# Kernel tuning notes

Hardware: AMD Instinct MI355X
Metric: run time of the kernel (lower is better)

The kernel has to match this reference:

```python
import jax, jax.numpy as jnp
import numpy as np

B, N, C = 128, 320, 768
H = 12
T = 64    # template tokens (8x8)
S = 256   # search tokens (16x16)


def setup_inputs() -> dict:
    key = jax.random.key(0)
    k1, k2, k3, k4 = jax.random.split(key, 4)
    return {
        "x1": jax.random.normal(k1, (B, N, C), dtype=jnp.float32),
        "x2": jax.random.normal(k2, (B, N, C), dtype=jnp.float32),
        "qkv_w": jax.random.normal(k3, (3 * C, C), dtype=jnp.float32) * 0.02,
        "proj_w": jax.random.normal(k4, (C, C), dtype=jnp.float32) * 0.02,
        "proj_b": jnp.zeros((C,), dtype=jnp.float32),
    }


def reference(x1, x2, qkv_w, proj_w, proj_b):
    # concat template tokens from x1 with search tokens from x2
    x = jnp.concatenate([x1[:, :T, :], x2[:, T:, :]], axis=1)  # [B, N, C]
    b, n, c = x.shape
    d = c // H
    scale = d ** -0.5

    qkv = (x @ qkv_w.T).reshape(b, n, 3, H, d).transpose(2, 0, 3, 1, 4)  # [3,B,H,N,D]
    q, k, v = qkv[0], qkv[1], qkv[2]

    # template -> template self-attention
    q_mt, k_mt, v_mt = q[:, :, :T], k[:, :, :T], v[:, :, :T]
    attn_mt = jax.nn.softmax(jnp.einsum('bhtd,bhsd->bhts', q_mt, k_mt) * scale, axis=-1)
    x_mt = jnp.einsum('bhts,bhsd->bhtd', attn_mt, v_mt).transpose(0, 2, 1, 3).reshape(b, T, c)

    # search -> all cross+self attention
    q_s = q[:, :, T:]
    attn_s = jax.nn.softmax(jnp.einsum('bhqd,bhkd->bhqk', q_s, k) * scale, axis=-1)
    x_s = jnp.einsum('bhqk,bhkd->bhqd', attn_s, v).transpose(0, 2, 1, 3).reshape(b, S, c)

    out = jnp.concatenate([x_mt, x_s], axis=1) @ proj_w.T + proj_b
    return out
```

## Files before the change

### kernel.cpp

```cpp
#include <hip/hip_runtime.h>
#include <hip/hip_bf16.h>
#include <stdint.h>

#define B_   128
#define N_   320
#define C_   768
#define H_   12
#define D_   64
#define NT_  (B_*N_)
#define K3_  (3*C_)
#define NKT  12
#define TE   (256*64)

typedef __attribute__((ext_vector_type(8))) __bf16 bf16x8;
typedef __attribute__((ext_vector_type(4))) float  f32x4;

__device__ __forceinline__ unsigned short f2bf(float f) {
  union { float f; unsigned u; } v; v.f = f;
  return (unsigned short)((v.u + 0x7fffu + ((v.u >> 16) & 1u)) >> 16);
}

__device__ __forceinline__ void gload16(const unsigned short* g, unsigned short* l) {
  __builtin_amdgcn_global_load_lds((const __attribute__((address_space(1))) void*)g,
                                   (__attribute__((address_space(3))) void*)l,
                                   16, 0, 0);
}

__global__ void prep_x(const float* __restrict__ x1, const float* __restrict__ x2,
                       unsigned short* __restrict__ xb) {
  const unsigned total4 = (unsigned)NT_ * C_ / 4;
  const unsigned stride = gridDim.x * blockDim.x;
  for (unsigned i = blockIdx.x * blockDim.x + threadIdx.x; i < total4; i += stride) {
    unsigned tok = i / (C_ / 4);
    unsigned n   = tok % N_;
    const float* src = (n < 64u) ? x1 : x2;
    float4 v = *(const float4*)(src + (size_t)i * 4u);
    ushort4 o;
    o.x = f2bf(v.x); o.y = f2bf(v.y); o.z = f2bf(v.z); o.w = f2bf(v.w);
    *(ushort4*)(xb + (size_t)i * 4u) = o;
  }
}

__global__ void prep_w(const float* __restrict__ qkv_w, const float* __restrict__ proj_w,
                       unsigned short* __restrict__ wq, unsigned short* __restrict__ wp) {
  const int QKV4 = (K3_ * C_) / 4;
  const int Q4   = (C_ * C_) / 4;
  const int P4   = (C_ * C_) / 4;
  int i = blockIdx.x * 256 + threadIdx.x;
  if (i < QKV4) {
    float s = (i < Q4) ? 0.125f : 1.0f;
    float4 v = *(const float4*)(qkv_w + (size_t)i * 4);
    ushort4 o;
    o.x = f2bf(v.x * s); o.y = f2bf(v.y * s); o.z = f2bf(v.z * s); o.w = f2bf(v.w * s);
    *(ushort4*)(wq + (size_t)i * 4) = o;
  } else if (i < QKV4 + P4) {
    int j = i - QKV4;
    float4 v = *(const float4*)(proj_w + (size_t)j * 4);
    ushort4 o;
    o.x = f2bf(v.x); o.y = f2bf(v.y); o.z = f2bf(v.z); o.w = f2bf(v.w);
    *(ushort4*)(wp + (size_t)j * 4) = o;
  }
}

#define BARR do { asm volatile("" ::: "memory"); __builtin_amdgcn_s_barrier(); asm volatile("" ::: "memory"); } while(0)
#define DSW  asm volatile("s_waitcnt lgkmcnt(0)" ::: "memory")
#define VMW(n) asm volatile("s_waitcnt vmcnt(" #n ")" ::: "memory")
#define PRIO1 __builtin_amdgcn_s_setprio(1)
#define PRIO0 __builtin_amdgcn_s_setprio(0)
#define RD(base, off) (*(const bf16x8*)((base) + (off)))

#define LDA_Q(QQ, PARX) do { \
    a_[0][0] = RD(bAk0, (PARX)*32768 + (QQ)*8192);        \
    a_[0][1] = RD(bAk1, (PARX)*32768 + (QQ)*8192);        \
    a_[1][0] = RD(bAk0, (PARX)*32768 + (QQ)*8192 + 2048); \
    a_[1][1] = RD(bAk1, (PARX)*32768 + (QQ)*8192 + 2048); } while(0)

#define LDB(PARX) do { \
    _Pragma("unroll") for (int nf = 0; nf < 4; ++nf) { \
      b_[0][nf] = RD(bBk0, (PARX)*32768 + nf*2048); \
      b_[1][nf] = RD(bBk1, (PARX)*32768 + nf*2048); } } while(0)

#define MFN(QQ) do { \
    _Pragma("unroll") for (int ks = 0; ks < 2; ++ks) \
    _Pragma("unroll") for (int f = 0; f < 2; ++f) \
    _Pragma("unroll") for (int nf = 0; nf < 4; ++nf) \
      acc[(QQ)*2+f][nf] = __builtin_amdgcn_mfma_f32_16x16x32_bf16(a_[f][ks], b_[ks][nf], acc[(QQ)*2+f][nf], 0, 0, 0); \
  } while(0)

#define MFS(QQ) do { \
    _Pragma("unroll") for (int ks = 0; ks < 2; ++ks) \
    _Pragma("unroll") for (int f = 0; f < 2; ++f) \
    _Pragma("unroll") for (int nf = 0; nf < 4; ++nf) \
      acc[(QQ)*2+f][nf] = __builtin_amdgcn_mfma_f32_16x16x32_bf16(b_[ks][nf], a_[f][ks], acc[(QQ)*2+f][nf], 0, 0, 0); \
  } while(0)

#define STGA_H0(PARX) do { gload16(gA00, dA + ((PARX)^1)*TE);        gload16(gA01, dA + ((PARX)^1)*TE + 512);  gA00 += 64; gA01 += 64; } while(0)
#define STGA_H1(PARX) do { gload16(gA10, dA + ((PARX)^1)*TE + 8192); gload16(gA11, dA + ((PARX)^1)*TE + 8704); gA10 += 64; gA11 += 64; } while(0)
#define STGB_H0(PARX) do { gload16(gB00, dB + (PARX)*TE);            gload16(gB01, dB + (PARX)*TE + 512);      gB00 += 64; gB01 += 64; } while(0)
#define STGB_H1(PARX) do { gload16(gB10, dB + (PARX)*TE + 8192);     gload16(gB11, dB + (PARX)*TE + 8704);     gB10 += 64; gB11 += 64; } while(0)

#define KTILE(MF, PARX, W1_, W3_) do { \
    LDA_Q(0, PARX); LDB(PARX); STGA_H0(PARX); \
    BARR; DSW; PRIO1; MF(0); PRIO0; BARR; \
    LDA_Q(1, PARX); STGA_H1(PARX); \
    BARR; DSW; PRIO1; MF(1); PRIO0; W1_; BARR; \
    LDA_Q(2, PARX); STGB_H0(PARX); \
    BARR; DSW; PRIO1; MF(2); PRIO0; BARR; \
    LDA_Q(3, PARX); STGB_H1(PARX); \
    BARR; DSW; PRIO1; MF(3); PRIO0; W3_; BARR; \
  } while(0)

#define RESETA do { \
    gA00 = Ag_ + (size_t)row0n*768 + offA00; gA01 = Ag_ + (size_t)row0n*768 + offA01; \
    gA10 = Ag_ + (size_t)row0n*768 + offA10; gA11 = Ag_ + (size_t)row0n*768 + offA11; } while(0)
#define RESETB do { \
    gB00 = Wg_ + (size_t)col0n*768 + offA00; gB01 = Wg_ + (size_t)col0n*768 + offA01; \
    gB10 = Wg_ + (size_t)col0n*768 + offA10; gB11 = Wg_ + (size_t)col0n*768 + offA11; } while(0)

#define TILE12(MF) do { \
    _Pragma("unroll 1") for (int tt = 0; tt < 5; ++tt) { \
      KTILE(MF, 0, VMW(8), VMW(6)); KTILE(MF, 1, VMW(8), VMW(6)); } \
    RESETB; KTILE(MF, 0, VMW(8), VMW(6)); \
    RESETA; KTILE(MF, 1, VMW(8), VMW(6)); \
  } while(0)

#define GEMM_SETUP \
  const int tid = threadIdx.x, lane = tid & 63, w = tid >> 6; \
  const int wr = w >> 2, wc = w & 3; \
  const int lr = lane & 15, kg = lane >> 4; \
  const int rr = lane >> 3; \
  const int sp = (lane & 7) ^ rr; \
  const char* bAk0 = (const char*)As + wr*4096 + lr*128 + ((0*4 + kg) ^ (lr & 7))*16; \
  const char* bAk1 = (const char*)As + wr*4096 + lr*128 + ((1*4 + kg) ^ (lr & 7))*16; \
  const char* bBk0 = (const char*)Bs + wc*8192 + lr*128 + ((0*4 + kg) ^ (lr & 7))*16; \
  const char* bBk1 = (const char*)Bs + wc*8192 + lr*128 + ((1*4 + kg) ^ (lr & 7))*16; \
  const size_t offA00 = (size_t)(w*16 + rr)*768 + sp*8; \
  const size_t offA01 = offA00 + (size_t)8*768; \
  const size_t offA10 = offA00 + (size_t)128*768; \
  const size_t offA11 = offA01 + (size_t)128*768; \
  unsigned short* dA = As + w*1024; \
  unsigned short* dB = Bs + w*1024; \
  const unsigned short *gA00, *gA01, *gA10, *gA11, *gB00, *gB01, *gB10, *gB11;

#define GEMM_PROLOGUE(row0i, col0i) do { \
    gA00 = Ag_ + (size_t)(row0i)*768 + offA00 + 64;  gA01 = Ag_ + (size_t)(row0i)*768 + offA01 + 64; \
    gA10 = Ag_ + (size_t)(row0i)*768 + offA10 + 64;  gA11 = Ag_ + (size_t)(row0i)*768 + offA11 + 64; \
    gB00 = Wg_ + (size_t)(col0i)*768 + offA00 + 128; gB01 = Wg_ + (size_t)(col0i)*768 + offA01 + 128; \
    gB10 = Wg_ + (size_t)(col0i)*768 + offA10 + 128; gB11 = Wg_ + (size_t)(col0i)*768 + offA11 + 128; \
    gload16(gA00 - 64,  dA);              gload16(gA01 - 64,  dA + 512); \
    gload16(gA10 - 64,  dA + 8192);       gload16(gA11 - 64,  dA + 8704); \
    gload16(gB00 - 128, dB);              gload16(gB01 - 128, dB + 512); \
    gload16(gB10 - 128, dB + 8192);       gload16(gB11 - 128, dB + 8704); \
    gload16(gB00 - 64,  dB + TE);         gload16(gB01 - 64,  dB + TE + 512); \
    gload16(gB10 - 64,  dB + TE + 8192);  gload16(gB11 - 64,  dB + TE + 8704); \
    VMW(4); BARR; \
  } while(0)

#define ACC_ZERO do { \
    _Pragma("unroll") for (int mf = 0; mf < 8; ++mf) \
    _Pragma("unroll") for (int nf = 0; nf < 4; ++nf) acc[mf][nf] = vzero; } while(0)

__global__ void __launch_bounds__(512, 2) gemm_qkv(const unsigned short* __restrict__ A,
                                                   const unsigned short* __restrict__ W,
                                                   unsigned short* __restrict__ qb,
                                                   unsigned short* __restrict__ kb,
                                                   unsigned short* __restrict__ vb) {
  __shared__ __align__(16) unsigned short As[2 * TE];
  __shared__ __align__(16) unsigned short Bs[2 * TE];
  GEMM_SETUP
  const unsigned short* Ag_ = A;
  const unsigned short* Wg_ = W;
  const int wv = blockIdx.x / 80;
  const int lb = blockIdx.x - wv * 80;

  const f32x4 vzero = {0.f, 0.f, 0.f, 0.f};
  f32x4 acc[8][4];
  ACC_ZERO;
  bf16x8 a_[2][2], b_[2][4];

  {
    const int t0i = lb * 6;
    const int row0i = (t0i / 3) * 256, col0i = (wv * 3 + t0i % 3) * 256;
    GEMM_PROLOGUE(row0i, col0i);
  }

  if (wv != 2) {
    unsigned short* dst = (wv == 0) ? qb : kb;
#pragma unroll 1
    for (int j = 0; j < 6; ++j) {
      const int t = lb * 6 + j, tn = (j < 5) ? t + 1 : t;
      const int row0c = (t / 3) * 256, cb = (t % 3) * 256;
      const int row0n = (tn / 3) * 256, col0n = (wv * 3 + tn % 3) * 256;
      TILE12(MFS);
#pragma unroll
      for (int mf = 0; mf < 8; ++mf) {
        const int tok = row0c + (mf >> 1) * 64 + wr * 32 + (mf & 1) * 16 + lr;
        const unsigned bq = (unsigned)tok / 320u;
        const int tt2 = tok - (int)bq * 320;
#pragma unroll
        for (int nf = 0; nf < 4; ++nf) {
          const int nn = cb + wc * 64 + nf * 16 + kg * 4;
          const int h = nn >> 6, dd = nn & 63;
          ushort4 o;
          o.x = f2bf(acc[mf][nf][0]); o.y = f2bf(acc[mf][nf][1]);
          o.z = f2bf(acc[mf][nf][2]); o.w = f2bf(acc[mf][nf][3]);
          *(ushort4*)&dst[(size_t)((((int)bq * 12 + h) * 320 + tt2) * 64 + dd)] = o;
        }
      }
      ACC_ZERO;
    }
  } else {
#pragma unroll 1
    for (int j = 0; j < 6; ++j) {
      const int t = lb * 6 + j, tn = (j < 5) ? t + 1 : t;
      const int row0c = (t / 3) * 256, cb = (t % 3) * 256;
      const int row0n = (tn / 3) * 256, col0n = (wv * 3 + tn % 3) * 256;
      TILE12(MFN);
#pragma unroll
      for (int mf = 0; mf < 8; ++mf) {
        const int m0 = row0c + (mf >> 1) * 64 + wr * 32 + (mf & 1) * 16 + kg * 4;
        const unsigned bq = (unsigned)m0 / 320u;
        const int t0v = m0 - (int)bq * 320;
#pragma unroll
        for (int nf = 0; nf < 4; ++nf) {
          const int nn = cb + wc * 64 + nf * 16 + lr;
          const int h = nn >> 6, dd = nn & 63;
          ushort4 o;
          o.x = f2bf(acc[mf][nf][0]); o.y = f2bf(acc[mf][nf][1]);
          o.z = f2bf(acc[mf][nf][2]); o.w = f2bf(acc[mf][nf][3]);
          *(ushort4*)&vb[(size_t)(((((int)bq * 12 + h) * 64 + dd) * 320) + t0v)] = o;
        }
      }
      ACC_ZERO;
    }
  }
  asm volatile("s_waitcnt vmcnt(0) lgkmcnt(0)" ::: "memory");
}

__global__ void __launch_bounds__(256) attn(const unsigned short* __restrict__ qb,
                                            const unsigned short* __restrict__ kb,
                                            const unsigned short* __restrict__ vb,
                                            unsigned short* __restrict__ ab) {
  __shared__ __align__(16) unsigned short Ks[64 * 64];
  __shared__ __align__(16) unsigned short Vt[64 * 64];
  __shared__ __align__(16) unsigned short Pl[4 * 16 * 64];
  const int bid = blockIdx.x;
  const int qt = bid % 5, bh = bid / 5;
  const int tid = threadIdx.x, lane = tid & 63, w = tid >> 6;
  const int lr = lane & 15, kg = lane >> 4;

  const int qrow = qt * 64 + w * 16 + lr;
  const unsigned short* qptr = qb + (bh * 320 + qrow) * 64;
  const bf16x8 qa0 = *(const bf16x8*)(qptr + kg * 8);
  const bf16x8 qa1 = *(const bf16x8*)(qptr + 32 + kg * 8);

  f32x4 o[4] = {};
  float mrun[4] = {-1e30f, -1e30f, -1e30f, -1e30f};
  float lrun[4] = {0.f, 0.f, 0.f, 0.f};
  const int nchunk = (qt == 0) ? 1 : 5;

  const int c0 = w, c1 = w + 4;
  const int srow0 = c0 * 8 + (lane >> 3);
  const int srow1 = c1 * 8 + (lane >> 3);
  const int slot  = lane & 7;
  const int part0 = slot ^ (srow0 & 7);
  const int part1 = slot ^ (srow1 & 7);
  const unsigned short* kbase = kb + bh * 320 * 64;
  const unsigned short* vbase = vb + bh * 64 * 320;
  unsigned short* lk0 = &Ks[c0 * 512];
  unsigned short* lk1 = &Ks[c1 * 512];
  unsigned short* lv0 = &Vt[c0 * 512];
  unsigned short* lv1 = &Vt[c1 * 512];
  char* PwB = (char*)&Pl[w * 1024];

  for (int kc = 0; kc < nchunk; kc++) {
    gload16(kbase + (kc * 64 + srow0) * 64 + part0 * 8, lk0);
    gload16(kbase + (kc * 64 + srow1) * 64 + part1 * 8, lk1);
    gload16(vbase + srow0 * 320 + kc * 64 + part0 * 8, lv0);
    gload16(vbase + srow1 * 320 + kc * 64 + part1 * 8, lv1);
    __syncthreads();

    f32x4 s[4];
#pragma unroll
    for (int kt = 0; kt < 4; kt++) {
      const int key = kt * 16 + lr;
      const char* kr = (const char*)Ks + key * 128;
      const unsigned sw = (unsigned)((key & 7) << 4);
      bf16x8 k0 = *(const bf16x8*)(kr + ((kg * 16) ^ sw));
      bf16x8 k1 = *(const bf16x8*)(kr + ((64 + kg * 16) ^ sw));
      f32x4 z = {0.f, 0.f, 0.f, 0.f};
      z = __builtin_amdgcn_mfma_f32_16x16x32_bf16(qa0, k0, z, 0, 0, 0);
      z = __builtin_amdgcn_mfma_f32_16x16x32_bf16(qa1, k1, z, 0, 0, 0);
      s[kt] = z;
    }

#pragma unroll
    for (int r = 0; r < 4; r++) {
      float rm = fmaxf(fmaxf(s[0][r], s[1][r]), fmaxf(s[2][r], s[3][r]));
      rm = fmaxf(rm, __shfl_xor(rm, 1));
      rm = fmaxf(rm, __shfl_xor(rm, 2));
      rm = fmaxf(rm, __shfl_xor(rm, 4));
      rm = fmaxf(rm, __shfl_xor(rm, 8));
      const float mn = fmaxf(mrun[r], rm);
      const float alpha = __expf(mrun[r] - mn);
      mrun[r] = mn;
      const int q = kg * 4 + r;
      char* prow = PwB + q * 128;
      const unsigned sw = (unsigned)((q & 7) << 4);
      float rs = 0.f;
#pragma unroll
      for (int kt = 0; kt < 4; kt++) {
        const float p = __expf(s[kt][r] - mn);
        rs += p;
        const int key = kt * 16 + lr;
        *(unsigned short*)(prow + ((key * 2) ^ sw)) = f2bf(p);
      }
      rs += __shfl_xor(rs, 1);
      rs += __shfl_xor(rs, 2);
      rs += __shfl_xor(rs, 4);
      rs += __shfl_xor(rs, 8);
      lrun[r] = lrun[r] * alpha + rs;
#pragma unroll
      for (int dt = 0; dt < 4; dt++) o[dt][r] *= alpha;
    }

    asm volatile("s_waitcnt lgkmcnt(0)" ::: "memory");

    {
      const char* par = (const char*)PwB + lr * 128;
      const unsigned swp = (unsigned)((lr & 7) << 4);
      bf16x8 p0 = *(const bf16x8*)(par + ((kg * 16) ^ swp));
      bf16x8 p1 = *(const bf16x8*)(par + ((64 + kg * 16) ^ swp));
#pragma unroll
      for (int dt = 0; dt < 4; dt++) {
        const int d = dt * 16 + lr;
        const char* vr = (const char*)Vt + d * 128;
        const unsigned swv = (unsigned)((d & 7) << 4);
        bf16x8 v0 = *(const bf16x8*)(vr + ((kg * 16) ^ swv));
        bf16x8 v1 = *(const bf16x8*)(vr + ((64 + kg * 16) ^ swv));
        o[dt] = __builtin_amdgcn_mfma_f32_16x16x32_bf16(p0, v0, o[dt], 0, 0, 0);
        o[dt] = __builtin_amdgcn_mfma_f32_16x16x32_bf16(p1, v1, o[dt], 0, 0, 0);
      }
    }
    __syncthreads();
  }

  const int b = bh / 12, h = bh - b * 12;
#pragma unroll
  for (int r = 0; r < 4; r++) {
    const float inv = 1.0f / lrun[r];
    const int token = b * 320 + qt * 64 + w * 16 + kg * 4 + r;
    unsigned short* orow = ab + token * 768 + h * 64;
#pragma unroll
    for (int dt = 0; dt < 4; dt++)
      orow[dt * 16 + lr] = f2bf(o[dt][r] * inv);
  }
}

__global__ void __launch_bounds__(512, 2) gemm_proj(const unsigned short* __restrict__ A,
                                                    const unsigned short* __restrict__ W,
                                                    const float* __restrict__ bias,
                                                    float* __restrict__ out) {
  __shared__ __align__(16) unsigned short As[2 * TE];
  __shared__ __align__(16) unsigned short Bs[2 * TE];
  GEMM_SETUP
  const unsigned short* Ag_ = A;
  const unsigned short* Wg_ = W;
  const int lb = blockIdx.x;

  const f32x4 vzero = {0.f, 0.f, 0.f, 0.f};
  f32x4 acc[8][4];
  ACC_ZERO;
  bf16x8 a_[2][2], b_[2][4];

  {
    const int t0i = lb * 2;
    const int row0i = (t0i / 3) * 256, col0i = (t0i % 3) * 256;
    GEMM_PROLOGUE(row0i, col0i);
  }

#pragma unroll 1
  for (int j = 0; j < 2; ++j) {
    const int t = lb * 2 + j, tn = (j < 1) ? t + 1 : t;
    const int row0c = (t / 3) * 256, col0c = (t % 3) * 256;
    const int row0n = (tn / 3) * 256, col0n = (tn % 3) * 256;
    TILE12(MFN);
#pragma unroll
    for (int nf = 0; nf < 4; ++nf) {
      const int nn = col0c + wc * 64 + nf * 16 + lr;
      const float bv = bias[nn];
#pragma unroll
      for (int mf = 0; mf < 8; ++mf) {
        const int m0 = row0c + (mf >> 1) * 64 + wr * 32 + (mf & 1) * 16 + kg * 4;
        float* po = out + (size_t)m0 * 768 + nn;
#pragma unroll
        for (int r = 0; r < 4; r++)
          po[(size_t)r * 768] = acc[mf][nf][r] + bv;
      }
    }
    ACC_ZERO;
  }
  asm volatile("s_waitcnt vmcnt(0) lgkmcnt(0)" ::: "memory");
}

extern "C" void kernel_launch(void* const* d_in, const int* in_sizes, int n_in,
                              void* d_out, int out_size, void* d_ws, size_t ws_size,
                              hipStream_t stream) {
  (void)in_sizes; (void)n_in; (void)out_size; (void)ws_size;
  const float* x1     = (const float*)d_in[0];
  const float* x2     = (const float*)d_in[1];
  const float* qkv_w  = (const float*)d_in[2];
  const float* proj_w = (const float*)d_in[3];
  const float* proj_b = (const float*)d_in[4];
  float* out = (float*)d_out;

  const size_t TOK = (size_t)NT_ * C_;
  unsigned short* xb = (unsigned short*)d_ws;
  unsigned short* qb = xb + TOK;
  unsigned short* kb = qb + TOK;
  unsigned short* vb = kb + TOK;
  unsigned short* ab = vb + TOK;
  unsigned short* wq = ab + TOK;
  unsigned short* wp = wq + (size_t)K3_ * C_;

  prep_x<<<8192, 256, 0, stream>>>(x1, x2, xb);
  prep_w<<<2304, 256, 0, stream>>>(qkv_w, proj_w, wq, wp);
  gemm_qkv<<<240, 512, 0, stream>>>(xb, wq, qb, kb, vb);
  attn<<<1536 * 5, 256, 0, stream>>>(qb, kb, vb, ab);
  gemm_proj<<<240, 512, 0, stream>>>(ab, wp, proj_b, out);
}
```

Measured before the change: 415.6 us.

## Restructure GEMM k-tile pipeline into two phases with fewer barriers

The per-k-tile schedule in both GEMM kernels changes from four quarter phases, each with two barriers, to two half phases with one barrier each. Each phase loads two A quarter-fragments into separate register arrays and issues all four A or B global-to-LDS loads together. The min-blocks-per-SM hint is dropped from the launch bounds so the compiler can use more registers for the extra fragments. The aim is less barrier and wait overhead and longer MFMA runs, at the cost of higher register pressure and likely lower occupancy.

```diff
diff --git a/kernel.cpp b/kernel.cpp
--- a/kernel.cpp
+++ b/kernel.cpp
@@ -69,45 +69,45 @@
 #define PRIO0 __builtin_amdgcn_s_setprio(0)
 #define RD(base, off) (*(const bf16x8*)((base) + (off)))
 
-#define LDA_Q(QQ, PARX) do { \
-    a_[0][0] = RD(bAk0, (PARX)*32768 + (QQ)*8192);        \
-    a_[0][1] = RD(bAk1, (PARX)*32768 + (QQ)*8192);        \
-    a_[1][0] = RD(bAk0, (PARX)*32768 + (QQ)*8192 + 2048); \
-    a_[1][1] = RD(bAk1, (PARX)*32768 + (QQ)*8192 + 2048); } while(0)
+#define LDA_Q(ARR, QQ, PARX) do { \
+    ARR[0][0] = RD(bAk0, (PARX)*32768 + (QQ)*8192);        \
+    ARR[0][1] = RD(bAk1, (PARX)*32768 + (QQ)*8192);        \
+    ARR[1][0] = RD(bAk0, (PARX)*32768 + (QQ)*8192 + 2048); \
+    ARR[1][1] = RD(bAk1, (PARX)*32768 + (QQ)*8192 + 2048); } while(0)
 
 #define LDB(PARX) do { \
     _Pragma("unroll") for (int nf = 0; nf < 4; ++nf) { \
       b_[0][nf] = RD(bBk0, (PARX)*32768 + nf*2048); \
       b_[1][nf] = RD(bBk1, (PARX)*32768 + nf*2048); } } while(0)
 
-#define MFN(QQ) do { \
+#define MFN(ARR, QQ) do { \
     _Pragma("unroll") for (int ks = 0; ks < 2; ++ks) \
     _Pragma("unroll") for (int f = 0; f < 2; ++f) \
     _Pragma("unroll") for (int nf = 0; nf < 4; ++nf) \
-      acc[(QQ)*2+f][nf] = __builtin_amdgcn_mfma_f32_16x16x32_bf16(a_[f][ks], b_[ks][nf], acc[(QQ)*2+f][nf], 0, 0, 0); \
+      acc[(QQ)*2+f][nf] = __builtin_amdgcn_mfma_f32_16x16x32_bf16(ARR[f][ks], b_[ks][nf], acc[(QQ)*2+f][nf], 0, 0, 0); \
   } while(0)
 
-#define MFS(QQ) do { \
+#define MFS(ARR, QQ) do { \
     _Pragma("unroll") for (int ks = 0; ks < 2; ++ks) \
     _Pragma("unroll") for (int f = 0; f < 2; ++f) \
     _Pragma("unroll") for (int nf = 0; nf < 4; ++nf) \
-      acc[(QQ)*2+f][nf] = __builtin_amdgcn_mfma_f32_16x16x32_bf16(b_[ks][nf], a_[f][ks], acc[(QQ)*2+f][nf], 0, 0, 0); \
+      acc[(QQ)*2+f][nf] = __builtin_amdgcn_mfma_f32_16x16x32_bf16(b_[ks][nf], ARR[f][ks], acc[(QQ)*2+f][nf], 0, 0, 0); \
   } while(0)
 
-#define STGA_H0(PARX) do { gload16(gA00, dA + ((PARX)^1)*TE);        gload16(gA01, dA + ((PARX)^1)*TE + 512);  gA00 += 64; gA01 += 64; } while(0)
-#define STGA_H1(PARX) do { gload16(gA10, dA + ((PARX)^1)*TE + 8192); gload16(gA11, dA + ((PARX)^1)*TE + 8704); gA10 += 64; gA11 += 64; } while(0)
-#define STGB_H0(PARX) do { gload16(gB00, dB + (PARX)*TE);            gload16(gB01, dB + (PARX)*TE + 512);      gB00 += 64; gB01 += 64; } while(0)
-#define STGB_H1(PARX) do { gload16(gB10, dB + (PARX)*TE + 8192);     gload16(gB11, dB + (PARX)*TE + 8704);     gB10 += 64; gB11 += 64; } while(0)
-
-#define KTILE(MF, PARX, W1_, W3_) do { \
-    LDA_Q(0, PARX); LDB(PARX); STGA_H0(PARX); \
-    BARR; DSW; PRIO1; MF(0); PRIO0; BARR; \
-    LDA_Q(1, PARX); STGA_H1(PARX); \
-    BARR; DSW; PRIO1; MF(1); PRIO0; W1_; BARR; \
-    LDA_Q(2, PARX); STGB_H0(PARX); \
-    BARR; DSW; PRIO1; MF(2); PRIO0; BARR; \
-    LDA_Q(3, PARX); STGB_H1(PARX); \
-    BARR; DSW; PRIO1; MF(3); PRIO0; W3_; BARR; \
+#define STGA4(PARX) do { \
+    gload16(gA00, dA + ((PARX)^1)*TE);        gload16(gA01, dA + ((PARX)^1)*TE + 512);  \
+    gload16(gA10, dA + ((PARX)^1)*TE + 8192); gload16(gA11, dA + ((PARX)^1)*TE + 8704); \
+    gA00 += 64; gA01 += 64; gA10 += 64; gA11 += 64; } while(0)
+#define STGB4(PARX) do { \
+    gload16(gB00, dB + (PARX)*TE);        gload16(gB01, dB + (PARX)*TE + 512);  \
+    gload16(gB10, dB + (PARX)*TE + 8192); gload16(gB11, dB + (PARX)*TE + 8704); \
+    gB00 += 64; gB01 += 64; gB10 += 64; gB11 += 64; } while(0)
+
+#define KT2(MF, PARX, S0_, S1_) do { \
+    LDA_Q(aL_, 0, PARX); LDA_Q(aH_, 1, PARX); LDB(PARX); S0_; \
+    DSW; PRIO1; MF(aL_, 0); MF(aH_, 1); PRIO0; BARR; \
+    LDA_Q(aL_, 2, PARX); LDA_Q(aH_, 3, PARX); S1_; \
+    DSW; PRIO1; MF(aL_, 2); MF(aH_, 3); PRIO0; VMW(4); BARR; \
   } while(0)
 
 #define RESETA do { \
@@ -119,9 +119,11 @@
 
 #define TILE12(MF) do { \
     _Pragma("unroll 1") for (int tt = 0; tt < 5; ++tt) { \
-      KTILE(MF, 0, VMW(8), VMW(6)); KTILE(MF, 1, VMW(8), VMW(6)); } \
-    RESETB; KTILE(MF, 0, VMW(8), VMW(6)); \
-    RESETA; KTILE(MF, 1, VMW(8), VMW(6)); \
+      KT2(MF, 0, STGA4(0), STGB4(0)); \
+      KT2(MF, 1, STGA4(1), STGB4(1)); \
+    } \
+    KT2(MF, 0, STGA4(0), { RESETB; STGB4(0); }); \
+    KT2(MF, 1, { RESETA; STGA4(1); }, STGB4(1)); \
   } while(0)
 
 #define GEMM_SETUP \
@@ -160,11 +162,11 @@
     _Pragma("unroll") for (int mf = 0; mf < 8; ++mf) \
     _Pragma("unroll") for (int nf = 0; nf < 4; ++nf) acc[mf][nf] = vzero; } while(0)
 
-__global__ void __launch_bounds__(512, 2) gemm_qkv(const unsigned short* __restrict__ A,
-                                                   const unsigned short* __restrict__ W,
-                                                   unsigned short* __restrict__ qb,
-                                                   unsigned short* __restrict__ kb,
-                                                   unsigned short* __restrict__ vb) {
+__global__ void __launch_bounds__(512) gemm_qkv(const unsigned short* __restrict__ A,
+                                                const unsigned short* __restrict__ W,
+                                                unsigned short* __restrict__ qb,
+                                                unsigned short* __restrict__ kb,
+                                                unsigned short* __restrict__ vb) {
   __shared__ __align__(16) unsigned short As[2 * TE];
   __shared__ __align__(16) unsigned short Bs[2 * TE];
   GEMM_SETUP
@@ -176,7 +178,7 @@
   const f32x4 vzero = {0.f, 0.f, 0.f, 0.f};
   f32x4 acc[8][4];
   ACC_ZERO;
-  bf16x8 a_[2][2], b_[2][4];
+  bf16x8 aL_[2][2], aH_[2][2], b_[2][4];
 
   {
     const int t0i = lb * 6;
@@ -357,10 +359,10 @@
   }
 }
 
-__global__ void __launch_bounds__(512, 2) gemm_proj(const unsigned short* __restrict__ A,
-                                                    const unsigned short* __restrict__ W,
-                                                    const float* __restrict__ bias,
-                                                    float* __restrict__ out) {
+__global__ void __launch_bounds__(512) gemm_proj(const unsigned short* __restrict__ A,
+                                                 const unsigned short* __restrict__ W,
+                                                 const float* __restrict__ bias,
+                                                 float* __restrict__ out) {
   __shared__ __align__(16) unsigned short As[2 * TE];
   __shared__ __align__(16) unsigned short Bs[2 * TE];
   GEMM_SETUP
@@ -371,7 +373,7 @@
   const f32x4 vzero = {0.f, 0.f, 0.f, 0.f};
   f32x4 acc[8][4];
   ACC_ZERO;
-  bf16x8 a_[2][2], b_[2][4];
+  bf16x8 aL_[2][2], aH_[2][2], b_[2][4];
 
   {
     const int t0i = lb * 2;
```

Result: faster. 406.9 us (-2.1%).
